# Optimization experiments

Measured on AMD Instinct MI355X. Metric: run time of the kernel, lower is better.

Reference implementation:

```python
import jax, jax.numpy as jnp
import numpy as np

D, H, O, E, K = 512, 2048, 512, 8, 2
CF = 1.0  # capacity_factor


def setup_inputs() -> dict:
    key = jax.random.key(0)
    ks = jax.random.split(key, 4)
    s = lambda k, shape, sc: jax.random.normal(k, shape, jnp.float32) * sc
    return {
        "x": s(ks[0], (8, 2048, D), 1.0),
        "gate_w": s(ks[1], (D, E), D ** -0.5),
        "gate_b": jnp.zeros((E,), jnp.float32),
        "w1": s(ks[2], (E, D, H), D ** -0.5),
        "b1": jnp.zeros((E, H), jnp.float32),
        "w2": s(ks[3], (E, H, O), H ** -0.5),
        "b2": jnp.zeros((E, O), jnp.float32),
    }


def _moe(x, gate_w, gate_b, w1, b1, w2, b2):
    orig = x.shape
    xf = x.reshape(-1, orig[-1])            # [N, D]
    N = xf.shape[0]
    capacity = max(int((N / E) * CF), 4)    # static (shape-derived)

    logits = xf @ gate_w + gate_b           # [N, E]
    gate_probs = jax.nn.softmax(logits, axis=-1)
    topk_p, topk_i = jax.lax.top_k(gate_probs, K)          # [N, K]
    norm_p = topk_p / topk_p.sum(-1, keepdims=True)        # [N, K]

    hot = jax.nn.one_hot(topk_i, E, dtype=xf.dtype)        # [N, K, E]
    mask = hot.sum(1)                                      # [N, E] in {0,1} (top-k indices unique)
    w_te = (norm_p[..., None] * hot).sum(1)                # [N, E] routing weight per token/expert

    def dispatch(m):
        # m: [N] 0/1 mask for one expert; keep first `capacity` tokens in token order
        cs = jnp.cumsum(m)
        keep = (m > 0) & (cs <= capacity)
        idx = jnp.argsort(jnp.where(keep, 0, 1), stable=True)[:capacity]  # kept tokens first, in order
        valid = jnp.arange(capacity) < keep.sum()
        return idx, valid

    idx, valid = jax.vmap(dispatch)(mask.T)                # idx: [E, cap], valid: [E, cap]

    gathered = xf[idx]                                     # [E, cap, D]
    h = jax.nn.gelu(jnp.einsum('ecd,edh->ech', gathered, w1) + b1[:, None, :], approximate=False)
    out = jnp.einsum('ech,eho->eco', h, w2) + b2[:, None, :]  # [E, cap, O]

    wg = w_te[idx, jnp.arange(E)[:, None]]                 # [E, cap] gate weight per dispatched token
    contrib = out * (wg * valid.astype(out.dtype))[..., None]
    combined = jnp.zeros((N, O), out.dtype).at[idx.reshape(-1)].add(contrib.reshape(-1, O))
    return combined.reshape(*orig[:-1], O), gate_probs


def reference(x, gate_w, gate_b, w1, b1, w2, b2):
    return _moe(x, gate_w, gate_b, w1, b1, w2, b2)
```

## Files before the change

kernel.cpp:

```cpp
#include <hip/hip_runtime.h>
#include <hip/hip_bf16.h>

#define NTOK 16384
#define DDIM 512
#define HDIM 2048
#define ODIM 512
#define NE 8
#define CAP 2048

typedef __attribute__((ext_vector_type(8))) short short8v;
typedef __attribute__((ext_vector_type(4))) short short4v;
typedef __attribute__((ext_vector_type(8))) unsigned short ushort8v;
typedef __attribute__((ext_vector_type(4))) float f32x4;

static __device__ __forceinline__ unsigned short f2bf(float f) {
  __hip_bfloat16 h = __float2bfloat16(f);
  return __builtin_bit_cast(unsigned short, h);
}

#define GLOAD_LDS16(gp, lp)                                               \
  __builtin_amdgcn_global_load_lds(                                       \
      (const __attribute__((address_space(1))) void*)(gp),                \
      (__attribute__((address_space(3))) void*)(lp), 16, 0, 0)

__global__ void k_transpose_cvt(const float* __restrict__ src,
                                __hip_bfloat16* __restrict__ dst, int R, int C) {
  __shared__ float tile[32][33];
  int e = blockIdx.z;
  size_t base = (size_t)e * R * C;
  int c0 = blockIdx.x * 32, r0 = blockIdx.y * 32;
  int tx = threadIdx.x, ty = threadIdx.y;
#pragma unroll
  for (int i = 0; i < 32; i += 8)
    tile[ty + i][tx] = src[base + (size_t)(r0 + ty + i) * C + c0 + tx];
  __syncthreads();
#pragma unroll
  for (int i = 0; i < 32; i += 8)
    dst[base + (size_t)(c0 + ty + i) * R + r0 + tx] = __float2bfloat16(tile[tx][ty + i]);
}

__global__ void k_gate(const float* __restrict__ x, const float* __restrict__ gw,
                       const float* __restrict__ gb, float* __restrict__ gate_probs,
                       int2* __restrict__ tk_e, float2* __restrict__ tk_w,
                       int* __restrict__ token_slot) {
  __shared__ float gws[DDIM * 9];
  int tid = threadIdx.x;
  for (int i = tid; i < DDIM * NE; i += 256) {
    int d = i >> 3, e = i & 7;
    gws[d * 9 + e] = gw[i];
  }
  __syncthreads();
  int wid = tid >> 6, lane = tid & 63;
  int t = blockIdx.x * 4 + wid;
  const float* xr = x + (size_t)t * DDIM;
  float acc[NE] = {0.f, 0.f, 0.f, 0.f, 0.f, 0.f, 0.f, 0.f};
#pragma unroll
  for (int j = 0; j < 8; ++j) {
    float xv = xr[lane + 64 * j];
    const float* g = &gws[(lane + 64 * j) * 9];
#pragma unroll
    for (int e = 0; e < NE; ++e) acc[e] += xv * g[e];
  }
#pragma unroll
  for (int e = 0; e < NE; ++e) {
#pragma unroll
    for (int off = 32; off > 0; off >>= 1) acc[e] += __shfl_xor(acc[e], off, 64);
  }
  if (lane == 0) {
    float p[NE];
    float m = -1e30f;
#pragma unroll
    for (int e = 0; e < NE; ++e) { p[e] = acc[e] + gb[e]; m = fmaxf(m, p[e]); }
    float s = 0.f;
#pragma unroll
    for (int e = 0; e < NE; ++e) { p[e] = expf(p[e] - m); s += p[e]; }
    float inv = 1.f / s;
#pragma unroll
    for (int e = 0; e < NE; ++e) { p[e] *= inv; gate_probs[(size_t)t * NE + e] = p[e]; }
    int i1 = 0; float p1 = p[0];
#pragma unroll
    for (int e = 1; e < NE; ++e) if (p[e] > p1) { p1 = p[e]; i1 = e; }
    int i2 = -1; float p2 = -1e30f;
#pragma unroll
    for (int e = 0; e < NE; ++e) if (e != i1 && p[e] > p2) { p2 = p[e]; i2 = e; }
    float wsum = p1 + p2;
    tk_e[t] = make_int2(i1, i2);
    tk_w[t] = make_float2(p1 / wsum, p2 / wsum);
    token_slot[2 * t] = -1;
    token_slot[2 * t + 1] = -1;
  }
}

__global__ void k_dispatch(const int2* __restrict__ tk_e, int* __restrict__ token_slot,
                           int* __restrict__ expert_tokens) {
  int e = blockIdx.x;
  int tid = threadIdx.x;
  int lane = tid & 63, w = tid >> 6;
  __shared__ int wave_cnt[16];
  int base = 0;
  for (int chunk = 0; chunk < NTOK / 1024; ++chunk) {
    int t = chunk * 1024 + tid;
    int2 te = tk_e[t];
    int k = (te.x == e) ? 0 : ((te.y == e) ? 1 : -1);
    bool flag = (k >= 0);
    unsigned long long m = __ballot(flag);
    int pre = __popcll(m & ((1ull << lane) - 1ull));
    __syncthreads();
    if (lane == 0) wave_cnt[w] = __popcll(m);
    __syncthreads();
    int off = 0, total = 0;
#pragma unroll
    for (int i = 0; i < 16; ++i) {
      off += (i < w) ? wave_cnt[i] : 0;
      total += wave_cnt[i];
    }
    int rank = base + off + pre;
    if (flag && rank < CAP) {
      expert_tokens[e * CAP + rank] = t;
      token_slot[2 * t + k] = e * CAP + rank;
    }
    base += total;
  }
  int nvalid = base < CAP ? base : CAP;
  for (int s = nvalid + tid; s < CAP; s += 1024)
    expert_tokens[e * CAP + s] = 0;
}

__global__ void k_gather(const float* __restrict__ x,
                         const int* __restrict__ expert_tokens,
                         __hip_bfloat16* __restrict__ xg) {
  int tid = threadIdx.x, wid = tid >> 6, lane = tid & 63;
  int slot = blockIdx.x * 4 + wid;
  int tok = expert_tokens[slot];
  const float4* src = reinterpret_cast<const float4*>(x + (size_t)tok * DDIM) + lane * 2;
  float4 u = src[0], v = src[1];
  ushort8v o;
  o[0] = f2bf(u.x); o[1] = f2bf(u.y); o[2] = f2bf(u.z); o[3] = f2bf(u.w);
  o[4] = f2bf(v.x); o[5] = f2bf(v.y); o[6] = f2bf(v.z); o[7] = f2bf(v.w);
  *reinterpret_cast<ushort8v*>(xg + (size_t)slot * DDIM + lane * 8) = o;
}

static __device__ __forceinline__ float gelu_fast(float v) {
  float z = 1.5957691216057308f * (v + 0.044715f * v * v * v);
  return v / (1.f + __expf(-z));
}

template <bool GELU, typename OutT>
__global__ __launch_bounds__(256) void k_gemm(
    const __hip_bfloat16* __restrict__ A, const __hip_bfloat16* __restrict__ B,
    const float* __restrict__ bias, OutT* __restrict__ C, int K, int M) {
  __shared__ char lds[2][2][8192];
  int gx = gridDim.x, gy = gridDim.y;
  int lin = (blockIdx.z * gy + blockIdx.y) * gx + blockIdx.x;
  int total = gx * gy * (int)gridDim.z;
  int cpx = total >> 3;
  lin = (lin & 7) * cpx + (lin >> 3);
  int gxy = gx * gy;
  int e = lin / gxy;
  int rem = lin - e * gxy;
  int mt = rem / gx, nt = rem - mt * gx;

  const int m0 = mt * 128, n0 = nt * 128;
  const int tid = threadIdx.x;
  const int lane = tid & 63, wid = tid >> 6;
  const int wr = wid >> 1, wc = wid & 1;
  const int lrow = lane & 15, kseg = lane >> 4;

  const int r0 = tid >> 2;
  const int sc = (tid & 3) ^ ((r0 >> 1) & 3);
  const int cb0 = (tid & 192) * 16;
  const int cb1 = 4096 + cb0;
  const __hip_bfloat16* Ab = A + ((size_t)e * M + m0) * K;
  const __hip_bfloat16* Bb = B + ((size_t)e * CAP + n0) * K;

#define STAGE(buf, kk)                                                      \
  do {                                                                      \
    GLOAD_LDS16(Ab + (size_t)r0 * K + (kk) + sc * 8, lds[buf][0] + cb0);    \
    GLOAD_LDS16(Ab + (size_t)(r0 + 64) * K + (kk) + sc * 8, lds[buf][0] + cb1); \
    GLOAD_LDS16(Bb + (size_t)r0 * K + (kk) + sc * 8, lds[buf][1] + cb0);    \
    GLOAD_LDS16(Bb + (size_t)(r0 + 64) * K + (kk) + sc * 8, lds[buf][1] + cb1); \
  } while (0)

  f32x4 acc[4][4] = {};
  STAGE(0, 0);
  __syncthreads();
  int cur = 0;
  for (int k0 = 0; k0 < K; k0 += 32) {
    if (k0 + 32 < K) {
      if (cur) STAGE(0, k0 + 32); else STAGE(1, k0 + 32);
    }
    const char* AsB = lds[cur][0];
    const char* BsB = lds[cur][1];
    short8v a[4], b[4];
#pragma unroll
    for (int mm = 0; mm < 4; ++mm) {
      int rr = wr * 64 + mm * 16 + lrow;
      int ks = kseg ^ ((rr >> 1) & 3);
      a[mm] = *reinterpret_cast<const short8v*>(AsB + rr * 64 + ks * 16);
    }
#pragma unroll
    for (int nn = 0; nn < 4; ++nn) {
      int rr = wc * 64 + nn * 16 + lrow;
      int ks = kseg ^ ((rr >> 1) & 3);
      b[nn] = *reinterpret_cast<const short8v*>(BsB + rr * 64 + ks * 16);
    }
#pragma unroll
    for (int mm = 0; mm < 4; ++mm)
#pragma unroll
      for (int nn = 0; nn < 4; ++nn)
        acc[mm][nn] = __builtin_amdgcn_mfma_f32_16x16x32_bf16(
            a[mm], b[nn], acc[mm][nn], 0, 0, 0);
    __syncthreads();
    cur ^= 1;
  }
#undef STAGE

#pragma unroll
  for (int mm = 0; mm < 4; ++mm) {
    int mrow = m0 + wr * 64 + mm * 16 + kseg * 4;
    float4 bv = *reinterpret_cast<const float4*>(&bias[e * M + mrow]);
#pragma unroll
    for (int nn = 0; nn < 4; ++nn) {
      int token = n0 + wc * 64 + nn * 16 + lrow;
      float v0 = acc[mm][nn][0] + bv.x;
      float v1 = acc[mm][nn][1] + bv.y;
      float v2 = acc[mm][nn][2] + bv.z;
      float v3 = acc[mm][nn][3] + bv.w;
      if (GELU) {
        v0 = gelu_fast(v0); v1 = gelu_fast(v1);
        v2 = gelu_fast(v2); v3 = gelu_fast(v3);
      }
      OutT* cp = C + ((size_t)e * CAP + token) * M + mrow;
      if constexpr (__is_same(OutT, __hip_bfloat16)) {
        short4v o;
        o[0] = (short)f2bf(v0); o[1] = (short)f2bf(v1);
        o[2] = (short)f2bf(v2); o[3] = (short)f2bf(v3);
        *reinterpret_cast<short4v*>(cp) = o;
      } else {
        float4 o = {v0, v1, v2, v3};
        *reinterpret_cast<float4*>(cp) = o;
      }
    }
  }
}

__global__ void k_combine(const float* __restrict__ outbuf,
                          const int* __restrict__ token_slot,
                          const float2* __restrict__ tk_w,
                          float* __restrict__ comb) {
  int tid = threadIdx.x;
  int wid = tid >> 6, lane = tid & 63;
  int t = blockIdx.x * 4 + wid;
  int s0 = token_slot[2 * t], s1 = token_slot[2 * t + 1];
  float2 w = tk_w[t];
  float r[8] = {0.f, 0.f, 0.f, 0.f, 0.f, 0.f, 0.f, 0.f};
  if (s0 >= 0) {
    const float4* p = reinterpret_cast<const float4*>(outbuf + (size_t)s0 * ODIM + lane * 8);
    float4 a = p[0], b = p[1];
    r[0] += w.x * a.x; r[1] += w.x * a.y; r[2] += w.x * a.z; r[3] += w.x * a.w;
    r[4] += w.x * b.x; r[5] += w.x * b.y; r[6] += w.x * b.z; r[7] += w.x * b.w;
  }
  if (s1 >= 0) {
    const float4* p = reinterpret_cast<const float4*>(outbuf + (size_t)s1 * ODIM + lane * 8);
    float4 a = p[0], b = p[1];
    r[0] += w.y * a.x; r[1] += w.y * a.y; r[2] += w.y * a.z; r[3] += w.y * a.w;
    r[4] += w.y * b.x; r[5] += w.y * b.y; r[6] += w.y * b.z; r[7] += w.y * b.w;
  }
  float4* q = reinterpret_cast<float4*>(comb + (size_t)t * ODIM + lane * 8);
  float4 o0 = {r[0], r[1], r[2], r[3]};
  float4 o1 = {r[4], r[5], r[6], r[7]};
  q[0] = o0;
  q[1] = o1;
}

extern "C" void kernel_launch(void* const* d_in, const int* in_sizes, int n_in,
                              void* d_out, int out_size, void* d_ws, size_t ws_size,
                              hipStream_t stream) {
  const float* x      = (const float*)d_in[0];
  const float* gate_w = (const float*)d_in[1];
  const float* gate_b = (const float*)d_in[2];
  const float* w1     = (const float*)d_in[3];
  const float* b1     = (const float*)d_in[4];
  const float* w2     = (const float*)d_in[5];
  const float* b2     = (const float*)d_in[6];

  float* comb = (float*)d_out;
  float* gate_probs = comb + (size_t)NTOK * ODIM;

  char* ws = (char*)d_ws;
  __hip_bfloat16* w1t    = (__hip_bfloat16*)(ws);
  __hip_bfloat16* w2t    = (__hip_bfloat16*)(ws + 16777216);
  __hip_bfloat16* hbuf   = (__hip_bfloat16*)(ws + 33554432);
  __hip_bfloat16* xg     = (__hip_bfloat16*)(ws + 100663296);
  float*          outbuf = (float*)(ws + 100663296);
  int*   expert_tokens   = (int*)(ws + 134217728);
  int2*  tk_e            = (int2*)(ws + 134283264);
  float2* tk_w           = (float2*)(ws + 134414336);
  int*   token_slot      = (int*)(ws + 134545408);

  k_transpose_cvt<<<dim3(HDIM / 32, DDIM / 32, NE), dim3(32, 8), 0, stream>>>(w1, w1t, DDIM, HDIM);
  k_transpose_cvt<<<dim3(ODIM / 32, HDIM / 32, NE), dim3(32, 8), 0, stream>>>(w2, w2t, HDIM, ODIM);
  k_gate<<<NTOK / 4, 256, 0, stream>>>(x, gate_w, gate_b, gate_probs, tk_e, tk_w, token_slot);
  k_dispatch<<<NE, 1024, 0, stream>>>(tk_e, token_slot, expert_tokens);
  k_gather<<<NE * CAP / 4, 256, 0, stream>>>(x, expert_tokens, xg);
  k_gemm<true, __hip_bfloat16>
      <<<dim3(CAP / 128, HDIM / 128, NE), 256, 0, stream>>>(w1t, xg, b1, hbuf, DDIM, HDIM);
  k_gemm<false, float>
      <<<dim3(CAP / 128, ODIM / 128, NE), 256, 0, stream>>>(w2t, hbuf, b2, outbuf, HDIM, ODIM);
  k_combine<<<NTOK / 4, 256, 0, stream>>>(outbuf, token_slot, tk_w, comb);
}
```

Before: 179.8 us.

## Triple-buffer GEMM K-loop with explicit vmcnt waits and early prefetch issue

Replaces the double-buffered LDS pipeline in the expert GEMM with a three-stage ring buffer. Loads run two tiles ahead, and readiness is tracked with explicit s_waitcnt vmcnt counts and raw s_barrier calls instead of __syncthreads. The next stage's global-to-LDS loads are issued right after the fragments are read into registers, and the MFMA block runs at raised wave priority. The goal is to hide global-memory latency better, at the cost of 48KB of LDS per block, which may lower occupancy. It also depends on the hand-counted vmcnt values being correct.

```diff
diff --git a/kernel.cpp b/kernel.cpp
--- a/kernel.cpp
+++ b/kernel.cpp
@@ -149,7 +149,7 @@
 __global__ __launch_bounds__(256) void k_gemm(
     const __hip_bfloat16* __restrict__ A, const __hip_bfloat16* __restrict__ B,
     const float* __restrict__ bias, OutT* __restrict__ C, int K, int M) {
-  __shared__ char lds[2][2][8192];
+  __shared__ char lds[3][16384];
   int gx = gridDim.x, gy = gridDim.y;
   int lin = (blockIdx.z * gy + blockIdx.y) * gx + blockIdx.x;
   int total = gx * gy * (int)gridDim.z;
@@ -173,24 +173,27 @@
   const __hip_bfloat16* Ab = A + ((size_t)e * M + m0) * K;
   const __hip_bfloat16* Bb = B + ((size_t)e * CAP + n0) * K;
 
-#define STAGE(buf, kk)                                                      \
-  do {                                                                      \
-    GLOAD_LDS16(Ab + (size_t)r0 * K + (kk) + sc * 8, lds[buf][0] + cb0);    \
-    GLOAD_LDS16(Ab + (size_t)(r0 + 64) * K + (kk) + sc * 8, lds[buf][0] + cb1); \
-    GLOAD_LDS16(Bb + (size_t)r0 * K + (kk) + sc * 8, lds[buf][1] + cb0);    \
-    GLOAD_LDS16(Bb + (size_t)(r0 + 64) * K + (kk) + sc * 8, lds[buf][1] + cb1); \
+#define STAGE(buf, kk)                                                         \
+  do {                                                                         \
+    GLOAD_LDS16(Ab + (size_t)r0 * K + (kk) + sc * 8, lds[buf] + cb0);          \
+    GLOAD_LDS16(Ab + (size_t)(r0 + 64) * K + (kk) + sc * 8, lds[buf] + cb1);   \
+    GLOAD_LDS16(Bb + (size_t)r0 * K + (kk) + sc * 8, lds[buf] + 8192 + cb0);   \
+    GLOAD_LDS16(Bb + (size_t)(r0 + 64) * K + (kk) + sc * 8, lds[buf] + 8192 + cb1); \
   } while (0)
 
   f32x4 acc[4][4] = {};
+  const int T = K >> 5;
   STAGE(0, 0);
-  __syncthreads();
+  STAGE(1, 32);
+  STAGE(2, 64);
   int cur = 0;
-  for (int k0 = 0; k0 < K; k0 += 32) {
-    if (k0 + 32 < K) {
-      if (cur) STAGE(0, k0 + 32); else STAGE(1, k0 + 32);
-    }
-    const char* AsB = lds[cur][0];
-    const char* BsB = lds[cur][1];
+  for (int t = 0; t < T; ++t) {
+    if (t < T - 2)       asm volatile("s_waitcnt vmcnt(8)" ::: "memory");
+    else if (t == T - 2) asm volatile("s_waitcnt vmcnt(4)" ::: "memory");
+    else                 asm volatile("s_waitcnt vmcnt(0)" ::: "memory");
+    __builtin_amdgcn_s_barrier();
+    const char* AsB = lds[cur];
+    const char* BsB = lds[cur] + 8192;
     short8v a[4], b[4];
 #pragma unroll
     for (int mm = 0; mm < 4; ++mm) {
@@ -204,14 +207,19 @@
       int ks = kseg ^ ((rr >> 1) & 3);
       b[nn] = *reinterpret_cast<const short8v*>(BsB + rr * 64 + ks * 16);
     }
+    asm volatile("s_waitcnt lgkmcnt(0)" ::: "memory");
+    __builtin_amdgcn_sched_barrier(0);
+    __builtin_amdgcn_s_barrier();
+    if (t + 3 < T) STAGE(cur, (t + 3) << 5);
+    __builtin_amdgcn_s_setprio(1);
 #pragma unroll
     for (int mm = 0; mm < 4; ++mm)
 #pragma unroll
       for (int nn = 0; nn < 4; ++nn)
         acc[mm][nn] = __builtin_amdgcn_mfma_f32_16x16x32_bf16(
             a[mm], b[nn], acc[mm][nn], 0, 0, 0);
-    __syncthreads();
-    cur ^= 1;
+    __builtin_amdgcn_s_setprio(0);
+    cur = (cur == 2) ? 0 : cur + 1;
   }
 #undef STAGE
 
```

New measurement: 179.7 us. Within noise of the previous version (-0.1%).
